# Optimization experiments

Hardware: AMD Instinct MI355X
Metric: run time of the kernel (lower is better)

The kernel has to match this reference:

```python
import jax, jax.numpy as jnp
import numpy as np

K_PER_CLASS = 10
WINDOW = 7
MIN_MASS = 0.05
EPS = 1e-8


def _pool_sum(x, w):
    # sum-pool over last two dims, stride 1, zero padding w//2 (count_include_pad avg = sum / w^2)
    nd = x.ndim
    return jax.lax.reduce_window(
        x, 0.0, jax.lax.add,
        (1,) * (nd - 2) + (w, w),
        (1,) * nd,
        [(0, 0)] * (nd - 2) + [(w // 2, w // 2)] * 2,
    )


def _l2norm(x, axis):
    # matches torch F.normalize(p=2): x / max(||x||, 1e-12)
    return x / jnp.maximum(jnp.linalg.norm(x, axis=axis, keepdims=True), 1e-12)


def setup_inputs() -> dict:
    key = jax.random.key(0)
    k1, k2, k3 = jax.random.split(key, 3)
    feature_map = jax.random.normal(k1, (8, 512, 96, 96), dtype=jnp.float32)
    prototypes = jax.random.normal(k2, (80, 512), dtype=jnp.float32)
    pseudo_mask = jax.random.randint(k3, (8, 96, 96), 0, 9, dtype=jnp.int32)
    return {"feature_map": feature_map, "prototypes": prototypes, "pseudo_mask": pseudo_mask}


def reference(feature_map, prototypes, pseudo_mask):
    B, D, H, W = feature_map.shape
    K = K_PER_CLASS
    C = prototypes.shape[0] // K
    area = WINDOW * WINDOW

    Fn = _l2norm(feature_map, 1)                       # [B,D,H,W]
    Pn = _l2norm(prototypes, 1).reshape(C, K, D)       # [C,K,D]
    sim = jnp.einsum('bdhw,ckd->bckhw', Fn, Pn)        # [B,C,K,H,W]

    omega = (pseudo_mask[:, None] == (jnp.arange(C) + 1)[None, :, None, None]).astype(sim.dtype)  # [B,C,H,W]

    num = _pool_sum(sim * omega[:, :, None], WINDOW) / area   # [B,C,K,H,W]
    den = _pool_sum(omega, WINDOW) / area                      # [B,C,H,W]
    region = num / (den[:, :, None] + EPS)

    a = region.reshape(B, C, K, H * W).transpose(0, 1, 3, 2)   # [B,C,HW,K]
    valid = (den > MIN_MASS).reshape(B, C, H * W)
    V = valid.sum(-1)                                          # [B,C] int
    Vf = jnp.maximum(V, 1).astype(a.dtype)
    vm = valid[..., None].astype(a.dtype)

    mean = (a * vm).sum(2) / Vf[..., None]                     # [B,C,K]
    a_c = (a - mean[:, :, None]) * vm                          # zero out invalid rows
    nrm = jnp.sqrt((a_c * a_c).sum(2))                         # [B,C,K]
    a_n = a_c / (nrm[:, :, None] + EPS)

    gram = jnp.einsum('bcvk,bcvl->bckl', a_n, a_n) / Vf[..., None, None]  # [B,C,K,K]
    off = gram * (1.0 - jnp.eye(K, dtype=gram.dtype))
    loss_c = (off * off).sum((-1, -2)) / (K * (K - 1))         # [B,C]

    active = (omega.sum((-1, -2)) >= 1.0) & (V >= 2)           # mirrors skip conditions
    af = active.astype(loss_c.dtype)
    per_image = (loss_c * af).sum(-1) / jnp.maximum(af.sum(-1), 1.0)
    return per_image.sum() / B
```

## Files before the change

kernel.cpp:

```cpp
#include <hip/hip_runtime.h>
#include <cstdint>
#include <cstddef>

namespace {
constexpr int Bn = 8, Dn = 512, Hn = 96, Wn = 96, HWn = Hn * Wn;
constexpr int Cn = 8, Kn = 10, CKn = Cn * Kn;
constexpr int NPIX = Bn * HWn;
constexpr int NCHUNK = 4, DCH = Dn / NCHUNK;
constexpr int NMOM = 66;
constexpr float EPSF = 1e-8f;
constexpr float MINM = 0.05f;

constexpr size_t oPnT  = 0;
constexpr size_t oS    = oPnT + (size_t)Dn * CKn;
constexpr size_t oNumH = oS + (size_t)Bn * Kn * HWn;
constexpr size_t oPart = oNumH;
constexpr size_t oDenH = oNumH + (size_t)Bn * Cn * Kn * HWn;
constexpr size_t oMom  = oDenH + (size_t)Bn * Cn * HWn;
constexpr size_t oCnt  = oMom + 64 * NMOM;
constexpr size_t oEnd  = oCnt + 64;
}

__device__ __forceinline__ float wred64(float v) {
#pragma unroll
    for (int o = 32; o > 0; o >>= 1) v += __shfl_down(v, o, 64);
    return v;
}

__global__ __launch_bounds__(64) void k_protonorm(const float* __restrict__ P,
                                                  float* __restrict__ PnT) {
    int ck = blockIdx.x, lane = threadIdx.x;
    float v[8]; float ss = 0.f;
#pragma unroll
    for (int j = 0; j < 8; ++j) { v[j] = P[ck * Dn + lane + 64 * j]; ss += v[j] * v[j]; }
    ss = wred64(ss);
    ss = __shfl(ss, 0, 64);
    float inv = 1.0f / fmaxf(sqrtf(ss), 1e-12f);
#pragma unroll
    for (int j = 0; j < 8; ++j)
        PnT[(size_t)(lane + 64 * j) * CKn + ck] = v[j] * inv;
}

__global__ __launch_bounds__(256) void k_sim(const float* __restrict__ F,
                                             const float* __restrict__ PnT,
                                             const int* __restrict__ mask,
                                             float* __restrict__ part) {
    __shared__ float pch[64 * 96];
    const int tid = threadIdx.x;
    const int pix = blockIdx.x * 256 + tid;
    const int chunk = blockIdx.y;
    const int b = pix / HWn, hw = pix % HWn;

    const int m = mask[pix];
    const int cc = m > 0 ? m - 1 : 0;

    float acc[Kn]; float ss = 0.f;
#pragma unroll
    for (int k = 0; k < Kn; ++k) acc[k] = 0.f;

    for (int p = 0; p < DCH / 64; ++p) {
        const int dbase = chunk * DCH + p * 64;
        __syncthreads();
        for (int i = tid; i < 64 * CKn; i += 256) {
            int dd = i / CKn, ck = i % CKn;
            int c = ck / Kn, kk = ck % Kn;
            pch[dd * 96 + c * 12 + kk] = PnT[(size_t)(dbase + dd) * CKn + ck];
        }
        __syncthreads();
#pragma unroll 4
        for (int dd = 0; dd < 64; ++dd) {
            float f = F[(size_t)(b * Dn + dbase + dd) * HWn + hw];
            ss += f * f;
            const float4* p4 = (const float4*)&pch[dd * 96 + cc * 12];
            float4 pa = p4[0], pb = p4[1];
            float2 pc = *(const float2*)&pch[dd * 96 + cc * 12 + 8];
            acc[0] += f * pa.x; acc[1] += f * pa.y; acc[2] += f * pa.z; acc[3] += f * pa.w;
            acc[4] += f * pb.x; acc[5] += f * pb.y; acc[6] += f * pb.z; acc[7] += f * pb.w;
            acc[8] += f * pc.x; acc[9] += f * pc.y;
        }
    }
#pragma unroll
    for (int k = 0; k < Kn; ++k)
        part[(size_t)(chunk * 11 + k) * NPIX + pix] = acc[k];
    part[(size_t)(chunk * 11 + 10) * NPIX + pix] = ss;
}

__global__ __launch_bounds__(256) void k_simred(const float* __restrict__ part,
                                                const int* __restrict__ mask,
                                                float* __restrict__ S,
                                                int* __restrict__ cnt) {
    __shared__ int hist[Cn];
    const int tid = threadIdx.x;
    const int pix = blockIdx.x * 256 + tid;
    if (tid < Cn) hist[tid] = 0;
    __syncthreads();

    float acc[Kn]; float ss = 0.f;
#pragma unroll
    for (int k = 0; k < Kn; ++k) acc[k] = 0.f;
#pragma unroll
    for (int ch = 0; ch < NCHUNK; ++ch) {
#pragma unroll
        for (int k = 0; k < Kn; ++k)
            acc[k] += part[(size_t)(ch * 11 + k) * NPIX + pix];
        ss += part[(size_t)(ch * 11 + 10) * NPIX + pix];
    }
    float inv = 1.0f / fmaxf(sqrtf(ss), 1e-12f);
    const int b = pix / HWn, hw = pix % HWn;
#pragma unroll
    for (int k = 0; k < Kn; ++k)
        S[(size_t)(b * Kn + k) * HWn + hw] = acc[k] * inv;

    const int m = mask[pix];
    if (m > 0) atomicAdd(&hist[m - 1], 1);
    __syncthreads();
    if (tid < Cn) atomicAdd(&cnt[(pix / HWn) * Cn + tid], hist[tid]);
}

__global__ __launch_bounds__(256) void k_hpool(const int* __restrict__ mask,
                                               const float* __restrict__ S,
                                               float* __restrict__ numH,
                                               float* __restrict__ denH) {
    const int i = blockIdx.x * 256 + threadIdx.x;
    const int hw = i % HWn;
    const int t = i / HWn;
    const int k2 = t % 5, bc = t / 5;
    const int c = bc % Cn, b = bc / Cn;
    const int k0 = 2 * k2;
    const int w = hw % Wn, row = hw - w;

    float den = 0.f, a0 = 0.f, a1 = 0.f;
#pragma unroll
    for (int dx = -3; dx <= 3; ++dx) {
        int ww = w + dx;
        if (ww < 0 || ww >= Wn) continue;
        int px = row + ww;
        bool hit = (mask[b * HWn + px] == c + 1);
        float s0 = S[(size_t)(b * Kn + k0) * HWn + px];
        float s1 = S[(size_t)(b * Kn + k0 + 1) * HWn + px];
        if (hit) { den += 1.f; a0 += s0; a1 += s1; }
    }
    numH[(size_t)(bc * Kn + k0) * HWn + hw] = a0;
    numH[(size_t)(bc * Kn + k0 + 1) * HWn + hw] = a1;
    if (k2 == 0) denH[(size_t)bc * HWn + hw] = den;
}

__global__ __launch_bounds__(256) void k_vpool(const float* __restrict__ numH,
                                               const float* __restrict__ denH,
                                               float* __restrict__ mom) {
    const int i = blockIdx.x * 256 + threadIdx.x;
    const int hw = i % HWn;
    const int bc = i / HWn;
    const int w = hw % Wn, h = hw / Wn;

    float den = 0.f;
    float n[Kn];
#pragma unroll
    for (int k = 0; k < Kn; ++k) n[k] = 0.f;

#pragma unroll
    for (int dy = -3; dy <= 3; ++dy) {
        int hh = h + dy;
        if (hh < 0 || hh >= Hn) continue;
        int px = hh * Wn + w;
        den += denH[(size_t)bc * HWn + px];
#pragma unroll
        for (int k = 0; k < Kn; ++k)
            n[k] += numH[(size_t)(bc * Kn + k) * HWn + px];
    }
    float dA = den * (1.0f / 49.0f);
    float inv = 1.0f / (dA + EPSF);
    float vm = (dA > MINM) ? 1.0f : 0.0f;
    float r[Kn];
#pragma unroll
    for (int k = 0; k < Kn; ++k) r[k] = n[k] * (1.0f / 49.0f) * inv * vm;

    __shared__ float red[4][NMOM];
    const int lane = threadIdx.x & 63, wv = threadIdx.x >> 6;
    {
        float x = wred64(vm);
        if (lane == 0) red[wv][0] = x;
    }
#pragma unroll
    for (int k = 0; k < Kn; ++k) {
        float x = wred64(r[k]);
        if (lane == 0) red[wv][1 + k] = x;
    }
    int p = 11;
#pragma unroll
    for (int k = 0; k < Kn; ++k) {
#pragma unroll
        for (int l = 0; l <= k; ++l, ++p) {
            float x = wred64(r[k] * r[l]);
            if (lane == 0) red[wv][p] = x;
        }
    }
    __syncthreads();
    for (int t = threadIdx.x; t < NMOM; t += 256)
        atomicAdd(&mom[bc * NMOM + t],
                  red[0][t] + red[1][t] + red[2][t] + red[3][t]);
}

__global__ __launch_bounds__(64) void k_final(const float* __restrict__ mom,
                                              const int* __restrict__ cnt,
                                              float* __restrict__ out) {
    const int bc = threadIdx.x;
    float mo[NMOM];
#pragma unroll
    for (int t = 0; t < NMOM; ++t) mo[t] = mom[bc * NMOM + t];
    const float V = mo[0];
    const float Vf = fmaxf(V, 1.0f);
    float Sk[Kn];
#pragma unroll
    for (int k = 0; k < Kn; ++k) Sk[k] = mo[1 + k];

    float M[55];
    {
        int p = 0;
#pragma unroll
        for (int k = 0; k < Kn; ++k)
#pragma unroll
            for (int l = 0; l <= k; ++l, ++p)
                M[p] = mo[11 + p] - Sk[k] * Sk[l] / Vf;
    }
    float nrm[Kn];
#pragma unroll
    for (int k = 0; k < Kn; ++k)
        nrm[k] = sqrtf(fmaxf(M[k * (k + 1) / 2 + k], 0.0f));
    float loss = 0.f;
    {
        int p = 0;
#pragma unroll
        for (int k = 0; k < Kn; ++k) {
#pragma unroll
            for (int l = 0; l <= k; ++l, ++p) {
                if (l == k) continue;
                float g = M[p] / ((nrm[k] + EPSF) * (nrm[l] + EPSF)) / Vf;
                loss += 2.0f * g * g;
            }
        }
    }
    loss *= 1.0f / (float)(Kn * (Kn - 1));
    bool act = (cnt[bc] >= 1) && (V >= 2.0f);
    float sl = act ? loss : 0.f;
    float sa = act ? 1.f : 0.f;
#pragma unroll
    for (int o = 4; o > 0; o >>= 1) {
        sl += __shfl_down(sl, o, 8);
        sa += __shfl_down(sa, o, 8);
    }
    __shared__ float pimg[Bn];
    if ((bc & 7) == 0) pimg[bc >> 3] = sl / fmaxf(sa, 1.0f);
    __syncthreads();
    if (bc == 0) {
        float tot = 0.f;
#pragma unroll
        for (int b = 0; b < Bn; ++b) tot += pimg[b];
        out[0] = tot / (float)Bn;
    }
}

extern "C" void kernel_launch(void* const* d_in, const int* in_sizes, int n_in,
                              void* d_out, int out_size, void* d_ws, size_t ws_size,
                              hipStream_t stream) {
    const float* F  = (const float*)d_in[0];
    const float* P  = (const float*)d_in[1];
    const int* mask = (const int*)d_in[2];
    float* ws = (float*)d_ws;
    float* out = (float*)d_out;

    hipMemsetAsync(ws + oMom, 0, (oEnd - oMom) * sizeof(float), stream);

    k_protonorm<<<CKn, 64, 0, stream>>>(P, ws + oPnT);
    k_sim<<<dim3(NPIX / 256, NCHUNK), 256, 0, stream>>>(F, ws + oPnT, mask, ws + oPart);
    k_simred<<<NPIX / 256, 256, 0, stream>>>(ws + oPart, mask, ws + oS, (int*)(ws + oCnt));
    k_hpool<<<Bn * Cn * 5 * HWn / 256, 256, 0, stream>>>(mask, ws + oS, ws + oNumH, ws + oDenH);
    k_vpool<<<Bn * Cn * HWn / 256, 256, 0, stream>>>(ws + oNumH, ws + oDenH, ws + oMom);
    k_final<<<1, 64, 0, stream>>>(ws + oMom, (const int*)(ws + oCnt), out);
}
```

Measured before the change: 308.4 us.

## Compute four outputs per thread in horizontal and vertical pooling kernels

The horizontal pool now has each thread produce four adjacent columns from a 10-wide strip and write float4 results. The vertical pool has each thread produce four adjacent rows of one column, reusing 10 loaded rows instead of 7 per output. Moments are accumulated in registers across the four outputs before a single set of 66 wave reductions, which cuts reduction work per pixel by four. The cost is more register pressure (40 accumulators plus 66 moments) and fewer threads in flight.

```diff
diff --git a/kernel.cpp b/kernel.cpp
--- a/kernel.cpp
+++ b/kernel.cpp
@@ -121,84 +121,120 @@
                                                const float* __restrict__ S,
                                                float* __restrict__ numH,
                                                float* __restrict__ denH) {
-    const int i = blockIdx.x * 256 + threadIdx.x;
-    const int hw = i % HWn;
-    const int t = i / HWn;
-    const int k2 = t % 5, bc = t / 5;
-    const int c = bc % Cn, b = bc / Cn;
+    const int t = blockIdx.x * 256 + threadIdx.x;
+    const int wg = t % 24;
+    int r = t / 24;
+    const int h = r % Hn; r /= Hn;
+    const int k2 = r % 5;
+    const int bc = r / 5;
+    const int c = bc & 7, b = bc >> 3;
     const int k0 = 2 * k2;
-    const int w = hw % Wn, row = hw - w;
-
-    float den = 0.f, a0 = 0.f, a1 = 0.f;
-#pragma unroll
-    for (int dx = -3; dx <= 3; ++dx) {
-        int ww = w + dx;
+    const int w0 = wg * 4;
+    const int rowb = b * HWn + h * Wn;
+    const float* S0 = &S[(size_t)(b * Kn + k0) * HWn + h * Wn];
+    const float* S1 = &S[(size_t)(b * Kn + k0 + 1) * HWn + h * Wn];
+
+    float a0[4] = {0.f, 0.f, 0.f, 0.f};
+    float a1[4] = {0.f, 0.f, 0.f, 0.f};
+    float dn[4] = {0.f, 0.f, 0.f, 0.f};
+
+#pragma unroll
+    for (int dc = -3; dc <= 6; ++dc) {
+        int ww = w0 + dc;
         if (ww < 0 || ww >= Wn) continue;
-        int px = row + ww;
-        bool hit = (mask[b * HWn + px] == c + 1);
-        float s0 = S[(size_t)(b * Kn + k0) * HWn + px];
-        float s1 = S[(size_t)(b * Kn + k0 + 1) * HWn + px];
-        if (hit) { den += 1.f; a0 += s0; a1 += s1; }
-    }
-    numH[(size_t)(bc * Kn + k0) * HWn + hw] = a0;
-    numH[(size_t)(bc * Kn + k0 + 1) * HWn + hw] = a1;
-    if (k2 == 0) denH[(size_t)bc * HWn + hw] = den;
+        float hv = (mask[rowb + ww] == c + 1) ? 1.0f : 0.0f;
+        float s0 = S0[ww] * hv;
+        float s1 = S1[ww] * hv;
+        const int olo = dc - 3 > 0 ? dc - 3 : 0;
+        const int ohi = dc + 3 < 3 ? dc + 3 : 3;
+#pragma unroll
+        for (int o = 0; o < 4; ++o) {
+            if (o < olo || o > ohi) continue;
+            a0[o] += s0; a1[o] += s1; dn[o] += hv;
+        }
+    }
+    float4* n0 = (float4*)&numH[(size_t)(bc * Kn + k0) * HWn + h * Wn + w0];
+    float4* n1 = (float4*)&numH[(size_t)(bc * Kn + k0 + 1) * HWn + h * Wn + w0];
+    *n0 = make_float4(a0[0], a0[1], a0[2], a0[3]);
+    *n1 = make_float4(a1[0], a1[1], a1[2], a1[3]);
+    if (k2 == 0)
+        *(float4*)&denH[(size_t)bc * HWn + h * Wn + w0] =
+            make_float4(dn[0], dn[1], dn[2], dn[3]);
 }
 
 __global__ __launch_bounds__(256) void k_vpool(const float* __restrict__ numH,
                                                const float* __restrict__ denH,
                                                float* __restrict__ mom) {
-    const int i = blockIdx.x * 256 + threadIdx.x;
-    const int hw = i % HWn;
-    const int bc = i / HWn;
-    const int w = hw % Wn, h = hw / Wn;
-
-    float den = 0.f;
-    float n[Kn];
-#pragma unroll
-    for (int k = 0; k < Kn; ++k) n[k] = 0.f;
-
-#pragma unroll
-    for (int dy = -3; dy <= 3; ++dy) {
-        int hh = h + dy;
+    const int t = blockIdx.x * 256 + threadIdx.x;
+    const int w = t % Wn;
+    int r = t / Wn;
+    const int hg = r % 24;
+    const int bc = r / 24;
+    const int h0 = hg * 4;
+
+    float nacc[4][Kn];
+    float dacc[4] = {0.f, 0.f, 0.f, 0.f};
+#pragma unroll
+    for (int o = 0; o < 4; ++o)
+#pragma unroll
+        for (int k = 0; k < Kn; ++k) nacc[o][k] = 0.f;
+
+#pragma unroll
+    for (int dr = -3; dr <= 6; ++dr) {
+        int hh = h0 + dr;
         if (hh < 0 || hh >= Hn) continue;
-        int px = hh * Wn + w;
-        den += denH[(size_t)bc * HWn + px];
+        const int olo = dr - 3 > 0 ? dr - 3 : 0;
+        const int ohi = dr + 3 < 3 ? dr + 3 : 3;
+        float dv = denH[(size_t)bc * HWn + hh * Wn + w];
+#pragma unroll
+        for (int o = 0; o < 4; ++o) {
+            if (o < olo || o > ohi) continue;
+            dacc[o] += dv;
+        }
+#pragma unroll
+        for (int k = 0; k < Kn; ++k) {
+            float nv = numH[(size_t)(bc * Kn + k) * HWn + hh * Wn + w];
+#pragma unroll
+            for (int o = 0; o < 4; ++o) {
+                if (o < olo || o > ohi) continue;
+                nacc[o][k] += nv;
+            }
+        }
+    }
+
+    float m[NMOM];
+#pragma unroll
+    for (int i = 0; i < NMOM; ++i) m[i] = 0.f;
+#pragma unroll
+    for (int o = 0; o < 4; ++o) {
+        float dA = dacc[o] * (1.0f / 49.0f);
+        float inv = 1.0f / (dA + EPSF);
+        float vm = (dA > MINM) ? 1.0f : 0.0f;
+        float rr[Kn];
 #pragma unroll
         for (int k = 0; k < Kn; ++k)
-            n[k] += numH[(size_t)(bc * Kn + k) * HWn + px];
-    }
-    float dA = den * (1.0f / 49.0f);
-    float inv = 1.0f / (dA + EPSF);
-    float vm = (dA > MINM) ? 1.0f : 0.0f;
-    float r[Kn];
-#pragma unroll
-    for (int k = 0; k < Kn; ++k) r[k] = n[k] * (1.0f / 49.0f) * inv * vm;
+            rr[k] = nacc[o][k] * (1.0f / 49.0f) * inv * vm;
+        m[0] += vm;
+#pragma unroll
+        for (int k = 0; k < Kn; ++k) m[1 + k] += rr[k];
+        int p = 11;
+#pragma unroll
+        for (int k = 0; k < Kn; ++k)
+#pragma unroll
+            for (int l = 0; l <= k; ++l, ++p) m[p] += rr[k] * rr[l];
+    }
 
     __shared__ float red[4][NMOM];
     const int lane = threadIdx.x & 63, wv = threadIdx.x >> 6;
-    {
-        float x = wred64(vm);
-        if (lane == 0) red[wv][0] = x;
-    }
-#pragma unroll
-    for (int k = 0; k < Kn; ++k) {
-        float x = wred64(r[k]);
-        if (lane == 0) red[wv][1 + k] = x;
-    }
-    int p = 11;
-#pragma unroll
-    for (int k = 0; k < Kn; ++k) {
-#pragma unroll
-        for (int l = 0; l <= k; ++l, ++p) {
-            float x = wred64(r[k] * r[l]);
-            if (lane == 0) red[wv][p] = x;
-        }
+#pragma unroll
+    for (int i = 0; i < NMOM; ++i) {
+        float x = wred64(m[i]);
+        if (lane == 0) red[wv][i] = x;
     }
     __syncthreads();
-    for (int t = threadIdx.x; t < NMOM; t += 256)
-        atomicAdd(&mom[bc * NMOM + t],
-                  red[0][t] + red[1][t] + red[2][t] + red[3][t]);
+    for (int i = threadIdx.x; i < NMOM; i += 256)
+        atomicAdd(&mom[bc * NMOM + i],
+                  red[0][i] + red[1][i] + red[2][i] + red[3][i]);
 }
 
 __global__ __launch_bounds__(64) void k_final(const float* __restrict__ mom,
@@ -207,7 +243,7 @@
     const int bc = threadIdx.x;
     float mo[NMOM];
 #pragma unroll
-    for (int t = 0; t < NMOM; ++t) mo[t] = mom[bc * NMOM + t];
+    for (int i = 0; i < NMOM; ++i) mo[i] = mom[bc * NMOM + i];
     const float V = mo[0];
     const float Vf = fmaxf(V, 1.0f);
     float Sk[Kn];
@@ -274,7 +310,8 @@
     k_protonorm<<<CKn, 64, 0, stream>>>(P, ws + oPnT);
     k_sim<<<dim3(NPIX / 256, NCHUNK), 256, 0, stream>>>(F, ws + oPnT, mask, ws + oPart);
     k_simred<<<NPIX / 256, 256, 0, stream>>>(ws + oPart, mask, ws + oS, (int*)(ws + oCnt));
-    k_hpool<<<Bn * Cn * 5 * HWn / 256, 256, 0, stream>>>(mask, ws + oS, ws + oNumH, ws + oDenH);
-    k_vpool<<<Bn * Cn * HWn / 256, 256, 0, stream>>>(ws + oNumH, ws + oDenH, ws + oMom);
+    k_hpool<<<Bn * Cn * 5 * Hn * 24 / 256, 256, 0, stream>>>(mask, ws + oS,
+                                                             ws + oNumH, ws + oDenH);
+    k_vpool<<<Bn * Cn * 24 * Wn / 256, 256, 0, stream>>>(ws + oNumH, ws + oDenH, ws + oMom);
     k_final<<<1, 64, 0, stream>>>(ws + oMom, (const int*)(ws + oCnt), out);
 }
```

Result: faster. 286.0 us (-7.2%).
